# Kernel optimization log

Hardware: AMD Instinct MI355X
Metric: run time of the kernel (lower is better)

The kernel has to match this reference:

```python
import jax, jax.numpy as jnp
import numpy as np

N = 4096
D_IN = 1024
D_Q = 1024
D_V = 1024

def setup_inputs() -> dict:
    key = jax.random.key(0)
    ks = jax.random.split(key, 8)
    # x scaled down a bit so exp() of raw (unstable, no max-subtract) scores stays finite,
    # matching the original module's numerics regime.
    x = jax.random.normal(ks[0], (N, D_IN), dtype=jnp.float32) * 0.02
    mask = jax.random.uniform(ks[1], (N, N), dtype=jnp.float32)
    s = 1.0 / np.sqrt(D_IN)
    Wq = jax.random.normal(ks[2], (D_IN, D_Q), dtype=jnp.float32) * s
    bq = jax.random.normal(ks[3], (D_Q,), dtype=jnp.float32) * 0.02
    Wk = jax.random.normal(ks[4], (D_IN, D_Q), dtype=jnp.float32) * s
    bk = jax.random.normal(ks[5], (D_Q,), dtype=jnp.float32) * 0.02
    Wv = jax.random.normal(ks[6], (D_IN, D_V), dtype=jnp.float32) * s
    bv = jax.random.normal(ks[7], (D_V,), dtype=jnp.float32) * 0.02
    return {"x": x, "mask": mask, "Wq": Wq, "bq": bq, "Wk": Wk, "bk": bk, "Wv": Wv, "bv": bv}

def reference(x, mask, Wq, bq, Wk, bk, Wv, bv):
    # Q, K, V projections (nn.Linear: x @ W + b, here W stored as [in, out])
    Q = x @ Wq + bq          # [N, Dq]
    K = x @ Wk + bk          # [N, Dq]
    V = x @ Wv + bv          # [N, Dv]
    scale = 1.0              # default scale in original forward
    scores = scale * (Q @ K.T)   # [N, N]
    scores = mask * scores       # elementwise multiplicative mask
    # Faithful to original (quirky) normalization:
    # exp(S) / sum(exp(S), axis=1)[None, :]  -> row-sums broadcast across ROWS
    e = jnp.exp(scores)                       # [N, N]
    denom = jnp.sum(e, axis=1)[None, :]       # [1, N]
    softmax = e / denom                       # [N, N]
    return softmax @ V                        # [N, Dv]
```

## Files before the change

kernel.cpp:

```cpp
#include <hip/hip_runtime.h>
#include <hip/hip_bf16.h>


#define N_TOK 4096
#define D_DIM 1024

typedef __bf16 bf16x8 __attribute__((ext_vector_type(8)));
typedef __bf16 bf16x4 __attribute__((ext_vector_type(4)));
typedef float  f32x4  __attribute__((ext_vector_type(4)));

typedef const __attribute__((address_space(1))) char g_char;
typedef __attribute__((address_space(3))) char lds_char;

__global__ void cvt_and_bias(const float* __restrict__ x, __bf16* __restrict__ xb,
                             const float* __restrict__ bq, const float* __restrict__ bk,
                             const float* __restrict__ bv, float* __restrict__ bcat) {
    int b = blockIdx.x;
    if (b < 4096) {
        int i = (b * 256 + threadIdx.x) * 4;
        float4 v = *(const float4*)(x + i);
        bf16x4 o;
        o.x = (__bf16)v.x; o.y = (__bf16)v.y;
        o.z = (__bf16)v.z; o.w = (__bf16)v.w;
        *(bf16x4*)(xb + i) = o;
    } else {
        int i = (b - 4096) * 256 + threadIdx.x;
        if (i < 1024) bcat[i] = bq[i];
        else if (i < 2048) bcat[i] = bk[i - 1024];
        else if (i < 3072) bcat[i] = bv[i - 2048];
    }
}

__global__ void transpose_w3(const float* __restrict__ Wq, const float* __restrict__ Wk,
                             const float* __restrict__ Wv, __bf16* __restrict__ outT) {
    const float* in = (blockIdx.z == 0) ? Wq : (blockIdx.z == 1) ? Wk : Wv;
    __bf16* oT = outT + (size_t)blockIdx.z * 1024 * 1024;
    __shared__ float t[64][65];
    const int c0 = blockIdx.x * 64, r0 = blockIdx.y * 64;
    const int tid = threadIdx.x;
#pragma unroll
    for (int k = 0; k < 16; k++) {
        int lin = tid + k * 256;
        int r = lin >> 6, c = lin & 63;
        t[r][c] = in[(size_t)(r0 + r) * 1024 + c0 + c];
    }
    __syncthreads();
#pragma unroll
    for (int k = 0; k < 16; k++) {
        int lin = tid + k * 256;
        int c = lin >> 6, r = lin & 63;
        oT[(size_t)(c0 + c) * 1024 + r0 + r] = (__bf16)t[r][c];
    }
}

__global__ void scale_transpose(const __bf16* __restrict__ V, int ldv,
                                const float* __restrict__ denom,
                                __bf16* __restrict__ VT) {
    __shared__ float t[64][65];
    __shared__ float rd[64];
    const int d0 = blockIdx.x * 64, j0 = blockIdx.y * 64;
    const int tid = threadIdx.x;
    if (tid < 64) rd[tid] = 1.0f / denom[j0 + tid];
    __syncthreads();
#pragma unroll
    for (int k = 0; k < 16; k++) {
        int lin = tid + k * 256;
        int j = lin >> 6, d = lin & 63;
        t[j][d] = (float)V[(size_t)(j0 + j) * ldv + d0 + d] * rd[j];
    }
    __syncthreads();
#pragma unroll
    for (int k = 0; k < 16; k++) {
        int lin = tid + k * 256;
        int d = lin >> 6, j = lin & 63;
        VT[(size_t)(d0 + d) * N_TOK + j0 + j] = (__bf16)t[j][d];
    }
}

template <int EPI, int TN>
__global__ __launch_bounds__(256, 2)
void gemm_nt(const __bf16* __restrict__ A, const __bf16* __restrict__ B,
             int lda, int ldb, int ldc, int K,
             const float* __restrict__ bias,
             const float* __restrict__ mask,
             __bf16* __restrict__ Cb, float* __restrict__ Cf,
             float* __restrict__ denom) {
    constexpr int NF = TN / 32;
    __shared__ __bf16 lA[128 * 64];
    __shared__ __bf16 lB[TN * 64];

    const int tid  = threadIdx.x;
    const int wave = tid >> 6;
    const int lane = tid & 63;
    const int quad = lane >> 4;
    const int l16  = lane & 15;
    const int m0 = blockIdx.y * 128;
    const int n0 = blockIdx.x * TN;
    const int wr = (wave >> 1) * 64;
    const int wc = (wave & 1) * (TN / 2);

    const size_t lda_b = (size_t)lda * 2;
    const size_t ldb_b = (size_t)ldb * 2;
    const int tr = tid >> 3;
    const int ts = ((tid & 7) ^ (tr & 7)) * 16;
    const char* gA = (const char*)A + (size_t)(m0 + tr) * lda_b + ts;
    const char* gB = (const char*)B + (size_t)(n0 + tr) * ldb_b + ts;
    const size_t pstepA = (size_t)32 * lda_b;
    const size_t pstepB = (size_t)32 * ldb_b;

    lds_char* lAp = (lds_char*)(void*)lA + wave * 1024;
    lds_char* lBp = (lds_char*)(void*)lB + wave * 1024;

    const int l7 = l16 & 7;
    const int rdA0 = ((wr + l16) * 128 + ((quad ^ l7) * 16)) >> 1;
    const int rdA1 = ((wr + l16) * 128 + (((4 + quad) ^ l7) * 16)) >> 1;
    const int rdB0 = ((wc + l16) * 128 + ((quad ^ l7) * 16)) >> 1;
    const int rdB1 = ((wc + l16) * 128 + (((4 + quad) ^ l7) * 16)) >> 1;

    f32x4 acc[4][NF];
#pragma unroll
    for (int i = 0; i < 4; i++)
#pragma unroll
        for (int j = 0; j < NF; j++) acc[i][j] = (f32x4){0.f, 0.f, 0.f, 0.f};

    for (int kt = 0; kt < K; kt += 64) {
#pragma unroll
        for (int c = 0; c < 4; c++)
            __builtin_amdgcn_global_load_lds((g_char*)(gA + c * pstepA),
                                             lAp + c * 4096, 16, 0, 0);
#pragma unroll
        for (int c = 0; c < NF; c++)
            __builtin_amdgcn_global_load_lds((g_char*)(gB + c * pstepB),
                                             lBp + c * 4096, 16, 0, 0);
        gA += 128;
        gB += 128;
        __syncthreads();

        bf16x8 af[4], bfr[NF];
#pragma unroll
        for (int i = 0; i < 4; i++) af[i] = *(const bf16x8*)&lA[rdA0 + i * 1024];
#pragma unroll
        for (int j = 0; j < NF; j++) bfr[j] = *(const bf16x8*)&lB[rdB0 + j * 1024];
#pragma unroll
        for (int i = 0; i < 4; i++)
#pragma unroll
            for (int j = 0; j < NF; j++)
                acc[i][j] = __builtin_amdgcn_mfma_f32_16x16x32_bf16(
                    af[i], bfr[j], acc[i][j], 0, 0, 0);
#pragma unroll
        for (int i = 0; i < 4; i++) af[i] = *(const bf16x8*)&lA[rdA1 + i * 1024];
#pragma unroll
        for (int j = 0; j < NF; j++) bfr[j] = *(const bf16x8*)&lB[rdB1 + j * 1024];
#pragma unroll
        for (int i = 0; i < 4; i++)
#pragma unroll
            for (int j = 0; j < NF; j++)
                acc[i][j] = __builtin_amdgcn_mfma_f32_16x16x32_bf16(
                    af[i], bfr[j], acc[i][j], 0, 0, 0);
        __syncthreads();
    }

#pragma unroll
    for (int i = 0; i < 4; i++) {
        const int rbase = m0 + wr + i * 16 + quad * 4;
        f32x4 rs = (f32x4){0.f, 0.f, 0.f, 0.f};
#pragma unroll
        for (int j = 0; j < NF; j++) {
            const int col = n0 + wc + j * 16 + l16;
            f32x4 v = acc[i][j];
            if (EPI == 0) {
                const float bb = bias[col];
#pragma unroll
                for (int r = 0; r < 4; r++)
                    Cb[(size_t)(rbase + r) * ldc + col] = (__bf16)(v[r] + bb);
            } else if (EPI == 1) {
#pragma unroll
                for (int r = 0; r < 4; r++) {
                    size_t idx = (size_t)(rbase + r) * ldc + col;
                    __bf16 eb = (__bf16)__expf(mask[idx] * v[r]);
                    Cb[idx] = eb;
                    rs[r] += (float)eb;
                }
            } else {
#pragma unroll
                for (int r = 0; r < 4; r++)
                    Cf[(size_t)(rbase + r) * ldc + col] = v[r];
            }
        }
        if (EPI == 1) {
#pragma unroll
            for (int m = 1; m < 16; m <<= 1) {
#pragma unroll
                for (int r = 0; r < 4; r++) rs[r] += __shfl_xor(rs[r], m, 64);
            }
            if (l16 == 0) {
#pragma unroll
                for (int r = 0; r < 4; r++) atomicAdd(&denom[rbase + r], rs[r]);
            }
        }
    }
}

extern "C" void kernel_launch(void* const* d_in, const int* in_sizes, int n_in,
                              void* d_out, int out_size, void* d_ws, size_t ws_size,
                              hipStream_t stream) {
    const float* x    = (const float*)d_in[0];
    const float* mask = (const float*)d_in[1];
    const float* Wq   = (const float*)d_in[2];
    const float* bq   = (const float*)d_in[3];
    const float* Wk   = (const float*)d_in[4];
    const float* bk   = (const float*)d_in[5];
    const float* Wv   = (const float*)d_in[6];
    const float* bv   = (const float*)d_in[7];
    float* out = (float*)d_out;
    char* ws = (char*)d_ws;

    const size_t MB = 1024 * 1024;
    __bf16* Eb    = (__bf16*)(ws + 0 * MB);
    __bf16* QKVb  = (__bf16*)(ws + 32 * MB);
    __bf16* xb    = (__bf16*)(ws + 56 * MB);
    __bf16* VsT   = xb;
    __bf16* WcatT = (__bf16*)(ws + 64 * MB);
    float*  bcat  = (float*)(ws + 70 * MB);
    float*  denom = (float*)(ws + 70 * MB + 64 * 1024);

    hipMemsetAsync(denom, 0, N_TOK * sizeof(float), stream);

    cvt_and_bias<<<4096 + 12, 256, 0, stream>>>(x, xb, bq, bk, bv, bcat);
    transpose_w3<<<dim3(16, 16, 3), 256, 0, stream>>>(Wq, Wk, Wv, WcatT);

    gemm_nt<0, 128><<<dim3(24, 32), 256, 0, stream>>>(
        xb, WcatT, D_DIM, D_DIM, 3 * D_DIM, D_DIM,
        bcat, nullptr, QKVb, nullptr, nullptr);

    const __bf16* Qb = QKVb;
    const __bf16* Kb = QKVb + D_DIM;
    gemm_nt<1, 128><<<dim3(32, 32), 256, 0, stream>>>(
        Qb, Kb, 3 * D_DIM, 3 * D_DIM, N_TOK, D_DIM,
        nullptr, mask, Eb, nullptr, denom);

    scale_transpose<<<dim3(16, 64), 256, 0, stream>>>(QKVb + 2048, 3 * D_DIM, denom, VsT);

    gemm_nt<2, 64><<<dim3(16, 32), 256, 0, stream>>>(
        Eb, VsT, N_TOK, N_TOK, D_DIM, N_TOK,
        nullptr, nullptr, nullptr, out, nullptr);
}
```

Baseline: 261.3 us.

## Quantize exp scores and scaled V to FP8 for the output GEMM

```diff
diff --git a/kernel.cpp b/kernel.cpp
--- a/kernel.cpp
+++ b/kernel.cpp
@@ -4,6 +4,7 @@
 
 #define N_TOK 4096
 #define D_DIM 1024
+#define VS_SCALE 131072.0f
 
 typedef __bf16 bf16x8 __attribute__((ext_vector_type(8)));
 typedef __bf16 bf16x4 __attribute__((ext_vector_type(4)));
@@ -11,6 +12,10 @@
 
 typedef const __attribute__((address_space(1))) char g_char;
 typedef __attribute__((address_space(3))) char lds_char;
+
+__device__ inline unsigned char f32_to_fp8(float f) {
+    return (unsigned char)(__builtin_amdgcn_cvt_pk_fp8_f32(f, f, 0, false) & 0xff);
+}
 
 __global__ void cvt_and_bias(const float* __restrict__ x, __bf16* __restrict__ xb,
                              const float* __restrict__ bq, const float* __restrict__ bk,
@@ -55,12 +60,12 @@
 
 __global__ void scale_transpose(const __bf16* __restrict__ V, int ldv,
                                 const float* __restrict__ denom,
-                                __bf16* __restrict__ VT) {
+                                unsigned char* __restrict__ VT8) {
     __shared__ float t[64][65];
     __shared__ float rd[64];
     const int d0 = blockIdx.x * 64, j0 = blockIdx.y * 64;
     const int tid = threadIdx.x;
-    if (tid < 64) rd[tid] = 1.0f / denom[j0 + tid];
+    if (tid < 64) rd[tid] = VS_SCALE / denom[j0 + tid];
     __syncthreads();
 #pragma unroll
     for (int k = 0; k < 16; k++) {
@@ -73,21 +78,20 @@
     for (int k = 0; k < 16; k++) {
         int lin = tid + k * 256;
         int d = lin >> 6, j = lin & 63;
-        VT[(size_t)(d0 + d) * N_TOK + j0 + j] = (__bf16)t[j][d];
-    }
-}
-
-template <int EPI, int TN>
+        VT8[(size_t)(d0 + d) * N_TOK + j0 + j] = f32_to_fp8(t[j][d]);
+    }
+}
+
+template <int EPI>
 __global__ __launch_bounds__(256, 2)
 void gemm_nt(const __bf16* __restrict__ A, const __bf16* __restrict__ B,
              int lda, int ldb, int ldc, int K,
              const float* __restrict__ bias,
              const float* __restrict__ mask,
-             __bf16* __restrict__ Cb, float* __restrict__ Cf,
+             __bf16* __restrict__ Cb, unsigned char* __restrict__ C8,
              float* __restrict__ denom) {
-    constexpr int NF = TN / 32;
     __shared__ __bf16 lA[128 * 64];
-    __shared__ __bf16 lB[TN * 64];
+    __shared__ __bf16 lB[128 * 64];
 
     const int tid  = threadIdx.x;
     const int wave = tid >> 6;
@@ -95,9 +99,9 @@
     const int quad = lane >> 4;
     const int l16  = lane & 15;
     const int m0 = blockIdx.y * 128;
-    const int n0 = blockIdx.x * TN;
+    const int n0 = blockIdx.x * 128;
     const int wr = (wave >> 1) * 64;
-    const int wc = (wave & 1) * (TN / 2);
+    const int wc = (wave & 1) * 64;
 
     const size_t lda_b = (size_t)lda * 2;
     const size_t ldb_b = (size_t)ldb * 2;
@@ -117,11 +121,11 @@
     const int rdB0 = ((wc + l16) * 128 + ((quad ^ l7) * 16)) >> 1;
     const int rdB1 = ((wc + l16) * 128 + (((4 + quad) ^ l7) * 16)) >> 1;
 
-    f32x4 acc[4][NF];
+    f32x4 acc[4][4];
 #pragma unroll
     for (int i = 0; i < 4; i++)
 #pragma unroll
-        for (int j = 0; j < NF; j++) acc[i][j] = (f32x4){0.f, 0.f, 0.f, 0.f};
+        for (int j = 0; j < 4; j++) acc[i][j] = (f32x4){0.f, 0.f, 0.f, 0.f};
 
     for (int kt = 0; kt < K; kt += 64) {
 #pragma unroll
@@ -129,32 +133,32 @@
             __builtin_amdgcn_global_load_lds((g_char*)(gA + c * pstepA),
                                              lAp + c * 4096, 16, 0, 0);
 #pragma unroll
-        for (int c = 0; c < NF; c++)
+        for (int c = 0; c < 4; c++)
             __builtin_amdgcn_global_load_lds((g_char*)(gB + c * pstepB),
                                              lBp + c * 4096, 16, 0, 0);
         gA += 128;
         gB += 128;
         __syncthreads();
 
-        bf16x8 af[4], bfr[NF];
+        bf16x8 af[4], bfr[4];
 #pragma unroll
         for (int i = 0; i < 4; i++) af[i] = *(const bf16x8*)&lA[rdA0 + i * 1024];
 #pragma unroll
-        for (int j = 0; j < NF; j++) bfr[j] = *(const bf16x8*)&lB[rdB0 + j * 1024];
+        for (int j = 0; j < 4; j++) bfr[j] = *(const bf16x8*)&lB[rdB0 + j * 1024];
 #pragma unroll
         for (int i = 0; i < 4; i++)
 #pragma unroll
-            for (int j = 0; j < NF; j++)
+            for (int j = 0; j < 4; j++)
                 acc[i][j] = __builtin_amdgcn_mfma_f32_16x16x32_bf16(
                     af[i], bfr[j], acc[i][j], 0, 0, 0);
 #pragma unroll
         for (int i = 0; i < 4; i++) af[i] = *(const bf16x8*)&lA[rdA1 + i * 1024];
 #pragma unroll
-        for (int j = 0; j < NF; j++) bfr[j] = *(const bf16x8*)&lB[rdB1 + j * 1024];
+        for (int j = 0; j < 4; j++) bfr[j] = *(const bf16x8*)&lB[rdB1 + j * 1024];
 #pragma unroll
         for (int i = 0; i < 4; i++)
 #pragma unroll
-            for (int j = 0; j < NF; j++)
+            for (int j = 0; j < 4; j++)
                 acc[i][j] = __builtin_amdgcn_mfma_f32_16x16x32_bf16(
                     af[i], bfr[j], acc[i][j], 0, 0, 0);
         __syncthreads();
@@ -165,7 +169,7 @@
         const int rbase = m0 + wr + i * 16 + quad * 4;
         f32x4 rs = (f32x4){0.f, 0.f, 0.f, 0.f};
 #pragma unroll
-        for (int j = 0; j < NF; j++) {
+        for (int j = 0; j < 4; j++) {
             const int col = n0 + wc + j * 16 + l16;
             f32x4 v = acc[i][j];
             if (EPI == 0) {
@@ -173,18 +177,14 @@
 #pragma unroll
                 for (int r = 0; r < 4; r++)
                     Cb[(size_t)(rbase + r) * ldc + col] = (__bf16)(v[r] + bb);
-            } else if (EPI == 1) {
+            } else {
 #pragma unroll
                 for (int r = 0; r < 4; r++) {
                     size_t idx = (size_t)(rbase + r) * ldc + col;
-                    __bf16 eb = (__bf16)__expf(mask[idx] * v[r]);
-                    Cb[idx] = eb;
-                    rs[r] += (float)eb;
+                    float e = __expf(mask[idx] * v[r]);
+                    C8[idx] = f32_to_fp8(e);
+                    rs[r] += e;
                 }
-            } else {
-#pragma unroll
-                for (int r = 0; r < 4; r++)
-                    Cf[(size_t)(rbase + r) * ldc + col] = v[r];
             }
         }
         if (EPI == 1) {
@@ -197,6 +197,93 @@
 #pragma unroll
                 for (int r = 0; r < 4; r++) atomicAdd(&denom[rbase + r], rs[r]);
             }
+        }
+    }
+}
+
+__global__ __launch_bounds__(256, 2)
+void gemm_out_fp8(const unsigned char* __restrict__ A,
+                  const unsigned char* __restrict__ B,
+                  float* __restrict__ C) {
+    __shared__ unsigned char lA[128 * 128];
+    __shared__ unsigned char lB[64 * 128];
+
+    const int tid  = threadIdx.x;
+    const int wave = tid >> 6;
+    const int lane = tid & 63;
+    const int quad = lane >> 4;
+    const int l16  = lane & 15;
+    const int m0 = blockIdx.y * 128;
+    const int n0 = blockIdx.x * 64;
+    const int wr = (wave >> 1) * 64;
+    const int wc = (wave & 1) * 32;
+
+    const int tr = tid >> 3;
+    const int ts = ((tid & 7) ^ (tr & 7)) * 16;
+    const char* gA = (const char*)A + (size_t)(m0 + tr) * N_TOK + ts;
+    const char* gB = (const char*)B + (size_t)(n0 + tr) * N_TOK + ts;
+    const size_t pstep = (size_t)32 * N_TOK;
+
+    lds_char* lAp = (lds_char*)(void*)lA + wave * 1024;
+    lds_char* lBp = (lds_char*)(void*)lB + wave * 1024;
+
+    const int l7 = l16 & 7;
+    const int qhi = quad >> 1, qlo = (quad & 1) * 8;
+    int rdA[4], rdB[4];
+#pragma unroll
+    for (int k = 0; k < 4; k++) {
+        rdA[k] = ((k * 2 + qhi) ^ l7) * 16 + qlo;
+        rdB[k] = rdA[k];
+    }
+
+    f32x4 acc[4][2];
+#pragma unroll
+    for (int i = 0; i < 4; i++)
+#pragma unroll
+        for (int j = 0; j < 2; j++) acc[i][j] = (f32x4){0.f, 0.f, 0.f, 0.f};
+
+    for (int kt = 0; kt < N_TOK; kt += 128) {
+#pragma unroll
+        for (int c = 0; c < 4; c++)
+            __builtin_amdgcn_global_load_lds((g_char*)(gA + c * pstep),
+                                             lAp + c * 4096, 16, 0, 0);
+#pragma unroll
+        for (int c = 0; c < 2; c++)
+            __builtin_amdgcn_global_load_lds((g_char*)(gB + c * pstep),
+                                             lBp + c * 4096, 16, 0, 0);
+        gA += 128;
+        gB += 128;
+        __syncthreads();
+
+#pragma unroll
+        for (int k = 0; k < 4; k++) {
+            long a[4], b[2];
+#pragma unroll
+            for (int i = 0; i < 4; i++)
+                a[i] = *(const long*)&lA[(wr + i * 16 + l16) * 128 + rdA[k]];
+#pragma unroll
+            for (int j = 0; j < 2; j++)
+                b[j] = *(const long*)&lB[(wc + j * 16 + l16) * 128 + rdB[k]];
+#pragma unroll
+            for (int i = 0; i < 4; i++)
+#pragma unroll
+                for (int j = 0; j < 2; j++)
+                    acc[i][j] = __builtin_amdgcn_mfma_f32_16x16x32_fp8_fp8(
+                        a[i], b[j], acc[i][j], 0, 0, 0);
+        }
+        __syncthreads();
+    }
+
+#pragma unroll
+    for (int i = 0; i < 4; i++) {
+#pragma unroll
+        for (int j = 0; j < 2; j++) {
+            const int col   = n0 + wc + j * 16 + l16;
+            const int rbase = m0 + wr + i * 16 + quad * 4;
+            f32x4 v = acc[i][j];
+#pragma unroll
+            for (int r = 0; r < 4; r++)
+                C[(size_t)(rbase + r) * D_DIM + col] = v[r] * (1.0f / VS_SCALE);
         }
     }
 }
@@ -216,32 +303,30 @@
     char* ws = (char*)d_ws;
 
     const size_t MB = 1024 * 1024;
-    __bf16* Eb    = (__bf16*)(ws + 0 * MB);
-    __bf16* QKVb  = (__bf16*)(ws + 32 * MB);
-    __bf16* xb    = (__bf16*)(ws + 56 * MB);
-    __bf16* VsT   = xb;
-    __bf16* WcatT = (__bf16*)(ws + 64 * MB);
-    float*  bcat  = (float*)(ws + 70 * MB);
-    float*  denom = (float*)(ws + 70 * MB + 64 * 1024);
+    unsigned char* E8   = (unsigned char*)(ws + 0 * MB);
+    __bf16* QKVb  = (__bf16*)(ws + 16 * MB);
+    __bf16* xb    = (__bf16*)(ws + 40 * MB);
+    unsigned char* VsT8 = (unsigned char*)xb;
+    __bf16* WcatT = (__bf16*)(ws + 48 * MB);
+    float*  bcat  = (float*)(ws + 54 * MB);
+    float*  denom = (float*)(ws + 54 * MB + 64 * 1024);
 
     hipMemsetAsync(denom, 0, N_TOK * sizeof(float), stream);
 
     cvt_and_bias<<<4096 + 12, 256, 0, stream>>>(x, xb, bq, bk, bv, bcat);
     transpose_w3<<<dim3(16, 16, 3), 256, 0, stream>>>(Wq, Wk, Wv, WcatT);
 
-    gemm_nt<0, 128><<<dim3(24, 32), 256, 0, stream>>>(
+    gemm_nt<0><<<dim3(24, 32), 256, 0, stream>>>(
         xb, WcatT, D_DIM, D_DIM, 3 * D_DIM, D_DIM,
         bcat, nullptr, QKVb, nullptr, nullptr);
 
     const __bf16* Qb = QKVb;
     const __bf16* Kb = QKVb + D_DIM;
-    gemm_nt<1, 128><<<dim3(32, 32), 256, 0, stream>>>(
+    gemm_nt<1><<<dim3(32, 32), 256, 0, stream>>>(
         Qb, Kb, 3 * D_DIM, 3 * D_DIM, N_TOK, D_DIM,
-        nullptr, mask, Eb, nullptr, denom);
-
-    scale_transpose<<<dim3(16, 64), 256, 0, stream>>>(QKVb + 2048, 3 * D_DIM, denom, VsT);
-
-    gemm_nt<2, 64><<<dim3(16, 32), 256, 0, stream>>>(
-        Eb, VsT, N_TOK, N_TOK, D_DIM, N_TOK,
-        nullptr, nullptr, nullptr, out, nullptr);
-}
+        nullptr, mask, nullptr, E8, denom);
+
+    scale_transpose<<<dim3(16, 64), 256, 0, stream>>>(QKVb + 2048, 3 * D_DIM, denom, VsT8);
+
+    gemm_out_fp8<<<dim3(16, 32), 256, 0, stream>>>(E8, VsT8, out);
+}
```

New measurement: 239.7 us. -8.3%, faster.

## Switch all three GEMMs to FP8 MFMA with offset-encoded exp and scaled V

Applied to the files above, without the earlier changes.

```diff
diff --git a/kernel.cpp b/kernel.cpp
--- a/kernel.cpp
+++ b/kernel.cpp
@@ -4,25 +4,27 @@
 
 #define N_TOK 4096
 #define D_DIM 1024
-
-typedef __bf16 bf16x8 __attribute__((ext_vector_type(8)));
-typedef __bf16 bf16x4 __attribute__((ext_vector_type(4)));
-typedef float  f32x4  __attribute__((ext_vector_type(4)));
+#define VS_SCALE 131072.0f
+
+typedef float f32x4 __attribute__((ext_vector_type(4)));
 
 typedef const __attribute__((address_space(1))) char g_char;
 typedef __attribute__((address_space(3))) char lds_char;
 
-__global__ void cvt_and_bias(const float* __restrict__ x, __bf16* __restrict__ xb,
+__device__ inline unsigned char f32_to_fp8(float f) {
+    return (unsigned char)(__builtin_amdgcn_cvt_pk_fp8_f32(f, f, 0, false) & 0xff);
+}
+
+__global__ void cvt_and_bias(const float* __restrict__ x, unsigned char* __restrict__ x8,
                              const float* __restrict__ bq, const float* __restrict__ bk,
                              const float* __restrict__ bv, float* __restrict__ bcat) {
     int b = blockIdx.x;
     if (b < 4096) {
         int i = (b * 256 + threadIdx.x) * 4;
         float4 v = *(const float4*)(x + i);
-        bf16x4 o;
-        o.x = (__bf16)v.x; o.y = (__bf16)v.y;
-        o.z = (__bf16)v.z; o.w = (__bf16)v.w;
-        *(bf16x4*)(xb + i) = o;
+        unsigned int lo = (unsigned int)__builtin_amdgcn_cvt_pk_fp8_f32(v.x, v.y, 0, false);
+        unsigned int pk = (unsigned int)__builtin_amdgcn_cvt_pk_fp8_f32(v.z, v.w, (int)lo, true);
+        *(unsigned int*)(x8 + i) = pk;
     } else {
         int i = (b - 4096) * 256 + threadIdx.x;
         if (i < 1024) bcat[i] = bq[i];
@@ -32,9 +34,9 @@
 }
 
 __global__ void transpose_w3(const float* __restrict__ Wq, const float* __restrict__ Wk,
-                             const float* __restrict__ Wv, __bf16* __restrict__ outT) {
+                             const float* __restrict__ Wv, unsigned char* __restrict__ outT) {
     const float* in = (blockIdx.z == 0) ? Wq : (blockIdx.z == 1) ? Wk : Wv;
-    __bf16* oT = outT + (size_t)blockIdx.z * 1024 * 1024;
+    unsigned char* oT = outT + (size_t)blockIdx.z * 1024 * 1024;
     __shared__ float t[64][65];
     const int c0 = blockIdx.x * 64, r0 = blockIdx.y * 64;
     const int tid = threadIdx.x;
@@ -49,45 +51,52 @@
     for (int k = 0; k < 16; k++) {
         int lin = tid + k * 256;
         int c = lin >> 6, r = lin & 63;
-        oT[(size_t)(c0 + c) * 1024 + r0 + r] = (__bf16)t[r][c];
-    }
-}
-
-__global__ void scale_transpose(const __bf16* __restrict__ V, int ldv,
+        oT[(size_t)(c0 + c) * 1024 + r0 + r] = f32_to_fp8(t[r][c]);
+    }
+}
+
+__global__ void scale_transpose(const __bf16* __restrict__ V,
                                 const float* __restrict__ denom,
-                                __bf16* __restrict__ VT) {
+                                unsigned char* __restrict__ VT8,
+                                float* __restrict__ colsum) {
     __shared__ float t[64][65];
     __shared__ float rd[64];
     const int d0 = blockIdx.x * 64, j0 = blockIdx.y * 64;
     const int tid = threadIdx.x;
-    if (tid < 64) rd[tid] = 1.0f / denom[j0 + tid];
+    const int lane = tid & 63;
+    if (tid < 64) rd[tid] = VS_SCALE / denom[j0 + tid];
     __syncthreads();
 #pragma unroll
     for (int k = 0; k < 16; k++) {
         int lin = tid + k * 256;
         int j = lin >> 6, d = lin & 63;
-        t[j][d] = (float)V[(size_t)(j0 + j) * ldv + d0 + d] * rd[j];
+        t[j][d] = (float)V[(size_t)(j0 + j) * D_DIM + d0 + d] * rd[j];
     }
     __syncthreads();
 #pragma unroll
     for (int k = 0; k < 16; k++) {
-        int lin = tid + k * 256;
-        int d = lin >> 6, j = lin & 63;
-        VT[(size_t)(d0 + d) * N_TOK + j0 + j] = (__bf16)t[j][d];
+        int d = (tid >> 6) + k * 4;
+        float val = t[lane][d];
+        VT8[(size_t)(d0 + d) * N_TOK + j0 + lane] = f32_to_fp8(val);
+#pragma unroll
+        for (int m = 1; m < 64; m <<= 1) val += __shfl_xor(val, m, 64);
+        if (lane == 0) atomicAdd(&colsum[d0 + d], val);
     }
 }
 
 template <int EPI, int TN>
 __global__ __launch_bounds__(256, 2)
-void gemm_nt(const __bf16* __restrict__ A, const __bf16* __restrict__ B,
-             int lda, int ldb, int ldc, int K,
-             const float* __restrict__ bias,
-             const float* __restrict__ mask,
-             __bf16* __restrict__ Cb, float* __restrict__ Cf,
-             float* __restrict__ denom) {
+void gemm_fp8(const unsigned char* __restrict__ A, const unsigned char* __restrict__ B,
+              int sA, int sB, int K,
+              const float* __restrict__ bias,
+              const float* __restrict__ mask,
+              unsigned char* __restrict__ QK8, __bf16* __restrict__ Vb,
+              unsigned char* __restrict__ F8, float* __restrict__ denom,
+              const float* __restrict__ colsum, float* __restrict__ C) {
     constexpr int NF = TN / 32;
-    __shared__ __bf16 lA[128 * 64];
-    __shared__ __bf16 lB[TN * 64];
+    constexpr int BP = TN / 32;
+    __shared__ unsigned char lA[128 * 128];
+    __shared__ unsigned char lB[TN * 128];
 
     const int tid  = threadIdx.x;
     const int wave = tid >> 6;
@@ -99,23 +108,21 @@
     const int wr = (wave >> 1) * 64;
     const int wc = (wave & 1) * (TN / 2);
 
-    const size_t lda_b = (size_t)lda * 2;
-    const size_t ldb_b = (size_t)ldb * 2;
     const int tr = tid >> 3;
     const int ts = ((tid & 7) ^ (tr & 7)) * 16;
-    const char* gA = (const char*)A + (size_t)(m0 + tr) * lda_b + ts;
-    const char* gB = (const char*)B + (size_t)(n0 + tr) * ldb_b + ts;
-    const size_t pstepA = (size_t)32 * lda_b;
-    const size_t pstepB = (size_t)32 * ldb_b;
+    const char* gA = (const char*)A + (size_t)(m0 + tr) * sA + ts;
+    const char* gB = (const char*)B + (size_t)(n0 + tr) * sB + ts;
+    const size_t pstepA = (size_t)32 * sA;
+    const size_t pstepB = (size_t)32 * sB;
 
     lds_char* lAp = (lds_char*)(void*)lA + wave * 1024;
     lds_char* lBp = (lds_char*)(void*)lB + wave * 1024;
 
     const int l7 = l16 & 7;
-    const int rdA0 = ((wr + l16) * 128 + ((quad ^ l7) * 16)) >> 1;
-    const int rdA1 = ((wr + l16) * 128 + (((4 + quad) ^ l7) * 16)) >> 1;
-    const int rdB0 = ((wc + l16) * 128 + ((quad ^ l7) * 16)) >> 1;
-    const int rdB1 = ((wc + l16) * 128 + (((4 + quad) ^ l7) * 16)) >> 1;
+    const int qhi = quad >> 1, qlo = (quad & 1) * 8;
+    int rd[4];
+#pragma unroll
+    for (int k = 0; k < 4; k++) rd[k] = ((k * 2 + qhi) ^ l7) * 16 + qlo;
 
     f32x4 acc[4][NF];
 #pragma unroll
@@ -123,40 +130,35 @@
 #pragma unroll
         for (int j = 0; j < NF; j++) acc[i][j] = (f32x4){0.f, 0.f, 0.f, 0.f};
 
-    for (int kt = 0; kt < K; kt += 64) {
+    for (int kt = 0; kt < K; kt += 128) {
 #pragma unroll
         for (int c = 0; c < 4; c++)
             __builtin_amdgcn_global_load_lds((g_char*)(gA + c * pstepA),
                                              lAp + c * 4096, 16, 0, 0);
 #pragma unroll
-        for (int c = 0; c < NF; c++)
+        for (int c = 0; c < BP; c++)
             __builtin_amdgcn_global_load_lds((g_char*)(gB + c * pstepB),
                                              lBp + c * 4096, 16, 0, 0);
         gA += 128;
         gB += 128;
         __syncthreads();
 
-        bf16x8 af[4], bfr[NF];
-#pragma unroll
-        for (int i = 0; i < 4; i++) af[i] = *(const bf16x8*)&lA[rdA0 + i * 1024];
-#pragma unroll
-        for (int j = 0; j < NF; j++) bfr[j] = *(const bf16x8*)&lB[rdB0 + j * 1024];
-#pragma unroll
-        for (int i = 0; i < 4; i++)
+#pragma unroll
+        for (int k = 0; k < 4; k++) {
+            long a[4], b[NF];
+#pragma unroll
+            for (int i = 0; i < 4; i++)
+                a[i] = *(const long*)&lA[(wr + i * 16 + l16) * 128 + rd[k]];
 #pragma unroll
             for (int j = 0; j < NF; j++)
-                acc[i][j] = __builtin_amdgcn_mfma_f32_16x16x32_bf16(
-                    af[i], bfr[j], acc[i][j], 0, 0, 0);
-#pragma unroll
-        for (int i = 0; i < 4; i++) af[i] = *(const bf16x8*)&lA[rdA1 + i * 1024];
-#pragma unroll
-        for (int j = 0; j < NF; j++) bfr[j] = *(const bf16x8*)&lB[rdB1 + j * 1024];
-#pragma unroll
-        for (int i = 0; i < 4; i++)
-#pragma unroll
-            for (int j = 0; j < NF; j++)
-                acc[i][j] = __builtin_amdgcn_mfma_f32_16x16x32_bf16(
-                    af[i], bfr[j], acc[i][j], 0, 0, 0);
+                b[j] = *(const long*)&lB[(wc + j * 16 + l16) * 128 + rd[k]];
+#pragma unroll
+            for (int i = 0; i < 4; i++)
+#pragma unroll
+                for (int j = 0; j < NF; j++)
+                    acc[i][j] = __builtin_amdgcn_mfma_f32_16x16x32_fp8_fp8(
+                        a[i], b[j], acc[i][j], 0, 0, 0);
+        }
         __syncthreads();
     }
 
@@ -170,21 +172,28 @@
             f32x4 v = acc[i][j];
             if (EPI == 0) {
                 const float bb = bias[col];
-#pragma unroll
-                for (int r = 0; r < 4; r++)
-                    Cb[(size_t)(rbase + r) * ldc + col] = (__bf16)(v[r] + bb);
+                if (n0 < 2048) {
+#pragma unroll
+                    for (int r = 0; r < 4; r++)
+                        QK8[(size_t)(rbase + r) * 2048 + col] = f32_to_fp8(v[r] + bb);
+                } else {
+#pragma unroll
+                    for (int r = 0; r < 4; r++)
+                        Vb[(size_t)(rbase + r) * 1024 + (col - 2048)] = (__bf16)(v[r] + bb);
+                }
             } else if (EPI == 1) {
 #pragma unroll
                 for (int r = 0; r < 4; r++) {
-                    size_t idx = (size_t)(rbase + r) * ldc + col;
-                    __bf16 eb = (__bf16)__expf(mask[idx] * v[r]);
-                    Cb[idx] = eb;
-                    rs[r] += (float)eb;
+                    size_t idx = (size_t)(rbase + r) * N_TOK + col;
+                    float e = __expf(mask[idx] * v[r]);
+                    F8[idx] = f32_to_fp8(e - 1.0f);
+                    rs[r] += e;
                 }
             } else {
 #pragma unroll
                 for (int r = 0; r < 4; r++)
-                    Cf[(size_t)(rbase + r) * ldc + col] = v[r];
+                    C[(size_t)(rbase + r) * D_DIM + col] =
+                        (v[r] + colsum[col]) * (1.0f / VS_SCALE);
             }
         }
         if (EPI == 1) {
@@ -216,32 +225,32 @@
     char* ws = (char*)d_ws;
 
     const size_t MB = 1024 * 1024;
-    __bf16* Eb    = (__bf16*)(ws + 0 * MB);
-    __bf16* QKVb  = (__bf16*)(ws + 32 * MB);
-    __bf16* xb    = (__bf16*)(ws + 56 * MB);
-    __bf16* VsT   = xb;
-    __bf16* WcatT = (__bf16*)(ws + 64 * MB);
-    float*  bcat  = (float*)(ws + 70 * MB);
-    float*  denom = (float*)(ws + 70 * MB + 64 * 1024);
-
-    hipMemsetAsync(denom, 0, N_TOK * sizeof(float), stream);
-
-    cvt_and_bias<<<4096 + 12, 256, 0, stream>>>(x, xb, bq, bk, bv, bcat);
-    transpose_w3<<<dim3(16, 16, 3), 256, 0, stream>>>(Wq, Wk, Wv, WcatT);
-
-    gemm_nt<0, 128><<<dim3(24, 32), 256, 0, stream>>>(
-        xb, WcatT, D_DIM, D_DIM, 3 * D_DIM, D_DIM,
-        bcat, nullptr, QKVb, nullptr, nullptr);
-
-    const __bf16* Qb = QKVb;
-    const __bf16* Kb = QKVb + D_DIM;
-    gemm_nt<1, 128><<<dim3(32, 32), 256, 0, stream>>>(
-        Qb, Kb, 3 * D_DIM, 3 * D_DIM, N_TOK, D_DIM,
-        nullptr, mask, Eb, nullptr, denom);
-
-    scale_transpose<<<dim3(16, 64), 256, 0, stream>>>(QKVb + 2048, 3 * D_DIM, denom, VsT);
-
-    gemm_nt<2, 64><<<dim3(16, 32), 256, 0, stream>>>(
-        Eb, VsT, N_TOK, N_TOK, D_DIM, N_TOK,
-        nullptr, nullptr, nullptr, out, nullptr);
-}
+    unsigned char* F8   = (unsigned char*)(ws + 0 * MB);
+    unsigned char* QK8  = (unsigned char*)(ws + 16 * MB);
+    __bf16*        Vb   = (__bf16*)(ws + 24 * MB);
+    unsigned char* x8   = (unsigned char*)(ws + 32 * MB);
+    unsigned char* VsT8 = x8;
+    unsigned char* W8T  = (unsigned char*)(ws + 36 * MB);
+    float* bcat   = (float*)(ws + 39 * MB);
+    float* denom  = (float*)(ws + 39 * MB + 16 * 1024);
+    float* colsum = (float*)(ws + 39 * MB + 32 * 1024);
+
+    hipMemsetAsync(denom, 0, 20 * 1024, stream);
+
+    cvt_and_bias<<<4096 + 12, 256, 0, stream>>>(x, x8, bq, bk, bv, bcat);
+    transpose_w3<<<dim3(16, 16, 3), 256, 0, stream>>>(Wq, Wk, Wv, W8T);
+
+    gemm_fp8<0, 128><<<dim3(24, 32), 256, 0, stream>>>(
+        x8, W8T, 1024, 1024, D_DIM,
+        bcat, nullptr, QK8, Vb, nullptr, nullptr, nullptr, nullptr);
+
+    gemm_fp8<1, 128><<<dim3(32, 32), 256, 0, stream>>>(
+        QK8, QK8 + 1024, 2048, 2048, D_DIM,
+        nullptr, mask, nullptr, nullptr, F8, denom, nullptr, nullptr);
+
+    scale_transpose<<<dim3(16, 64), 256, 0, stream>>>(Vb, denom, VsT8, colsum);
+
+    gemm_fp8<2, 64><<<dim3(16, 32), 256, 0, stream>>>(
+        F8, VsT8, 4096, 4096, N_TOK,
+        nullptr, nullptr, nullptr, nullptr, nullptr, nullptr, colsum, out);
+}
```

Result: no change. 259.6 us (-0.7%).
